# Optimization experiments

Hardware: AMD Instinct MI355X
Metric: run time of the kernel (lower is better)

Reference implementation:

```python
import jax, jax.numpy as jnp
import numpy as np

# Perfect-tree regularization of the recursive UpDownVec graph:
#   T tactics per internal node, S siblings per tactic, L levels, branching B = T*S.
T, S, L = 2, 4, 7
B = T * S
DIM = 128
EPS = 1.0  # epsilon in AggChildrenVec
SIZES = [B ** l for l in range(L)]          # nodes per level: 1, 8, ..., 262144
OFFS = np.concatenate([[0], np.cumsum(SIZES)])
N_TOTAL = int(OFFS[-1])                      # 299593


def setup_inputs() -> dict:
    key = jax.random.key(0)
    ks = jax.random.split(key, 12)
    sc = 1.0 / np.sqrt(DIM)
    return {
        "initial_vecs": jax.random.normal(ks[0], (N_TOTAL, DIM), jnp.float32),
        "Ws": jax.random.normal(ks[1], (DIM, DIM), jnp.float32) * sc,
        "bs": jax.random.normal(ks[2], (DIM,), jnp.float32) * sc,
        "Wc": jax.random.normal(ks[3], (DIM, DIM), jnp.float32) * sc,
        "bc": jax.random.normal(ks[4], (DIM,), jnp.float32) * sc,
        "Wx": jax.random.normal(ks[5], (DIM, DIM), jnp.float32) * sc,
        "bx": jax.random.normal(ks[6], (DIM,), jnp.float32) * sc,
        "Wf": jax.random.normal(ks[7], (DIM, 2 * DIM), jnp.float32) * sc,
        "bf": jax.random.normal(ks[8], (DIM,), jnp.float32) * sc,
        "Wh": jax.random.normal(ks[9], (1, DIM), jnp.float32) * sc,
        "bh": jax.random.normal(ks[10], (1,), jnp.float32) * sc,
    }


def reference(initial_vecs, Ws, bs, Wc, bc, Wx, bx, Wf, bf, Wh, bh):
    dim = initial_vecs.shape[-1]
    init = [initial_vecs[OFFS[l]:OFFS[l + 1]] for l in range(L)]  # static slices

    # ---- up_step (bottom-up): leaves -> root ----
    agg = [None] * L
    agg[L - 1] = init[L - 1]                                    # leaves: agg = initial
    for l in range(L - 2, -1, -1):
        ch = agg[l + 1].reshape(SIZES[l], T, S, dim)            # children agg vecs
        # AggSiblingsVec: mean over siblings of relu(linear)
        sib_h = jax.nn.relu(jnp.einsum('ntsd,ed->ntse', ch, Ws) + bs)
        sib_agg = sib_h.mean(axis=2)                            # [n, T, dim]
        # AggChildrenVec: node + eps * mean over tactics of relu(linear)
        ch_h = jax.nn.relu(jnp.einsum('ntd,ed->nte', sib_agg, Wc) + bc)
        agg[l] = init[l] + EPS * ch_h.mean(axis=1)

    # ---- down_step (top-down): root -> leaves ----
    ctx = [None] * L
    ctx[0] = jnp.ones((1, dim), initial_vecs.dtype)             # root context = ones
    for l in range(L - 1):
        # AggContextVec over cat([parent_ctx, other_siblings_agg]); mean is
        # order-invariant so set-based sibling gathering is reproduced exactly.
        h = jax.nn.relu(agg[l + 1] @ Wx.T + bx).reshape(SIZES[l], T, S, dim)
        sum_h = h.sum(axis=2)                                   # [n, T, dim]
        ctx_h = jax.nn.relu(ctx[l] @ Wx.T + bx)                 # [n, dim]
        child_ctx = (ctx_h[:, None, None, :] + sum_h[:, :, None, :] - h) / S
        ctx[l + 1] = child_ctx.reshape(SIZES[l + 1], dim)

    # ---- final_agg for every node ----
    ctx_all = jnp.concatenate(ctx, axis=0)                      # [N, dim]
    agg_all = jnp.concatenate(agg, axis=0)                      # [N, dim]
    x = jnp.concatenate([ctx_all, agg_all], axis=1)             # [N, 2*dim]
    x = jax.nn.relu(x @ Wf.T + bf)
    return x @ Wh.T + bh                                        # [N, 1]
```

## Files before the change

### kernel.cpp

```cpp
#include <hip/hip_runtime.h>
#include <stdint.h>

#define DIM 128

static constexpr long long NTOT = 299593LL;

using bf16x8 = __attribute__((ext_vector_type(8))) __bf16;
using f32x4  = __attribute__((ext_vector_type(4))) float;

__device__ __forceinline__ float relu(float x){ return x > 0.f ? x : 0.f; }
__device__ __forceinline__ __bf16 tobf(float x){ return (__bf16)x; }

__device__ __forceinline__ void mfma_acc(f32x4& acc, bf16x8 a, bf16x8 b){
    acc = __builtin_amdgcn_mfma_f32_16x16x32_bf16(a, b, acc, 0, 0, 0);
}

__device__ __forceinline__ int swz(int row, int col){
    return row*128 + (col ^ ((row & 7) << 3));
}

__global__ __launch_bounds__(256) void prep_kernel(
    const float* __restrict__ Ws, const float* __restrict__ Wc,
    const float* __restrict__ Wx, const float* __restrict__ Wf,
    __bf16* __restrict__ wfm, __bf16* __restrict__ ctx)
{
    int idx = blockIdx.x*256 + threadIdx.x;
    if (idx < 81920){
        int sel = idx >> 14;
        int d   = idx & 16383;
        int j = d & 7, ln = (d >> 3) & 63, f = d >> 9;
        int r = (f >> 2)*16 + (ln & 15);
        int c = (f & 3)*32 + (ln >> 4)*8 + j;
        float v;
        if      (sel == 0) v = Ws[r*128 + c];
        else if (sel == 1) v = Wc[r*128 + c];
        else if (sel == 2) v = Wx[r*128 + c];
        else if (sel == 3) v = Wf[r*256 + c];
        else               v = Wf[r*256 + 128 + c];
        wfm[idx] = tobf(v);
    } else if (idx < 82048){
        ctx[idx - 81920] = tobf(1.0f);
    }
}


__device__ __forceinline__ void up_level_task(
    const __bf16* __restrict__ lds_w,
    __bf16* __restrict__ sib,
    const float* __restrict__ init,
    const float* __restrict__ bsr, const float* __restrict__ bcr,
    __bf16* __restrict__ agg,
    long long task, long long cb, long long pb, long long n_par,
    int lane, int quad, int l15)
{
    const long long n_child = n_par*8;
    const long long c0 = task*64;
    bf16x8 af[4][4];
    #pragma unroll
    for (int tt = 0; tt < 4; ++tt){
        long long r = c0 + tt*16 + l15;
        if (r >= n_child) r = n_child - 1;
        const __bf16* p = agg + (cb + r)*DIM + quad*8;
        #pragma unroll
        for (int ks = 0; ks < 4; ++ks)
            af[tt][ks] = *(const bf16x8*)(p + ks*32);
    }
    #pragma unroll
    for (int h = 0; h < 2; ++h){
        f32x4 acc[2][8];
        #pragma unroll
        for (int u = 0; u < 2; ++u)
            #pragma unroll
            for (int i = 0; i < 8; ++i) acc[u][i] = f32x4{0.f,0.f,0.f,0.f};
        #pragma unroll
        for (int ks = 0; ks < 4; ++ks){
            #pragma unroll
            for (int nt = 0; nt < 8; ++nt){
                bf16x8 b = *(const bf16x8*)&lds_w[((nt*4+ks)<<9) + lane*8];
                mfma_acc(acc[0][nt], af[2*h+0][ks], b);
                mfma_acc(acc[1][nt], af[2*h+1][ks], b);
            }
        }
        #pragma unroll
        for (int u = 0; u < 2; ++u){
            const int row = (2*h+u)*4 + quad;
            #pragma unroll
            for (int nt = 0; nt < 8; ++nt){
                float b = bsr[nt];
                float s = relu(acc[u][nt][0]+b) + relu(acc[u][nt][1]+b)
                        + relu(acc[u][nt][2]+b) + relu(acc[u][nt][3]+b);
                sib[swz(row, nt*16 + l15)] = tobf(s*0.25f);
            }
        }
    }
    bf16x8 a2[4];
    #pragma unroll
    for (int ks = 0; ks < 4; ++ks)
        a2[ks] = *(const bf16x8*)&sib[swz(l15, ks*32 + quad*8)];
    f32x4 ac2[8];
    #pragma unroll
    for (int i = 0; i < 8; ++i) ac2[i] = f32x4{0.f,0.f,0.f,0.f};
    #pragma unroll
    for (int ks = 0; ks < 4; ++ks){
        #pragma unroll
        for (int nt = 0; nt < 8; ++nt){
            bf16x8 b = *(const bf16x8*)&lds_w[16384 + ((nt*4+ks)<<9) + lane*8];
            mfma_acc(ac2[nt], a2[ks], b);
        }
    }
    const long long p0l = task*8 + quad*2, p1l = p0l + 1;
    #pragma unroll
    for (int nt = 0; nt < 8; ++nt){
        int col = nt*16 + l15;
        float b = bcr[nt];
        float r0_ = relu(ac2[nt][0]+b), r1_ = relu(ac2[nt][1]+b);
        float r2_ = relu(ac2[nt][2]+b), r3_ = relu(ac2[nt][3]+b);
        if (p0l < n_par){
            long long gr = pb + p0l;
            agg[gr*DIM + col] = tobf(init[gr*DIM + col] + 0.5f*(r0_+r1_));
        }
        if (p1l < n_par){
            long long gr = pb + p1l;
            agg[gr*DIM + col] = tobf(init[gr*DIM + col] + 0.5f*(r2_+r3_));
        }
    }
}

__device__ __forceinline__ void down_level_task(
    const __bf16* __restrict__ lds_w,
    __bf16* __restrict__ ch,
    const float* __restrict__ bxr,
    const __bf16* __restrict__ agg, __bf16* __restrict__ ctx,
    long long task, long long pb, long long cb, long long n_par,
    int lane, int quad, int l15)
{
    const long long n_child = n_par*8;
    {
        long long p = task*16 + l15;
        if (p >= n_par) p = n_par - 1;
        bf16x8 ap[4];
        #pragma unroll
        for (int ks = 0; ks < 4; ++ks)
            ap[ks] = *(const bf16x8*)(ctx + (pb + p)*DIM + ks*32 + quad*8);
        f32x4 acp[8];
        #pragma unroll
        for (int i = 0; i < 8; ++i) acp[i] = f32x4{0.f,0.f,0.f,0.f};
        #pragma unroll
        for (int ks = 0; ks < 4; ++ks){
            #pragma unroll
            for (int nt = 0; nt < 8; ++nt){
                bf16x8 b = *(const bf16x8*)&lds_w[((nt*4+ks)<<9) + lane*8];
                mfma_acc(acp[nt], ap[ks], b);
            }
        }
        #pragma unroll
        for (int nt = 0; nt < 8; ++nt){
            float b = bxr[nt];
            #pragma unroll
            for (int rg = 0; rg < 4; ++rg)
                ch[swz(quad*4 + rg, nt*16 + l15)] = tobf(relu(acp[nt][rg] + b));
        }
    }
    #pragma unroll 1
    for (int ct = 0; ct < 8; ++ct){
        const long long ch0 = task*128 + ct*16;
        if (ch0 >= n_child) break;
        bf16x8 a[4];
        {
            long long r = ch0 + l15;
            if (r >= n_child) r = n_child - 1;
            const __bf16* p = agg + (cb + r)*DIM + quad*8;
            #pragma unroll
            for (int ks = 0; ks < 4; ++ks)
                a[ks] = *(const bf16x8*)(p + ks*32);
        }
        f32x4 acc[8];
        #pragma unroll
        for (int i = 0; i < 8; ++i) acc[i] = f32x4{0.f,0.f,0.f,0.f};
        #pragma unroll
        for (int ks = 0; ks < 4; ++ks){
            #pragma unroll
            for (int nt = 0; nt < 8; ++nt){
                bf16x8 b = *(const bf16x8*)&lds_w[((nt*4+ks)<<9) + lane*8];
                mfma_acc(acc[nt], a[ks], b);
            }
        }
        const long long rb = ch0 + quad*4;
        const int p_loc = ct*2 + (quad >> 1);
        #pragma unroll
        for (int nt = 0; nt < 8; ++nt){
            int col = nt*16 + l15;
            float b = bxr[nt];
            float h0 = relu(acc[nt][0]+b), h1 = relu(acc[nt][1]+b);
            float h2 = relu(acc[nt][2]+b), h3 = relu(acc[nt][3]+b);
            float s = h0 + h1 + h2 + h3;
            float chv = (float)ch[swz(p_loc, col)];
            if (rb   < n_child) ctx[(cb + rb  )*DIM + col] = tobf((chv + s - h0)*0.25f);
            if (rb+1 < n_child) ctx[(cb + rb+1)*DIM + col] = tobf((chv + s - h1)*0.25f);
            if (rb+2 < n_child) ctx[(cb + rb+2)*DIM + col] = tobf((chv + s - h2)*0.25f);
            if (rb+3 < n_child) ctx[(cb + rb+3)*DIM + col] = tobf((chv + s - h3)*0.25f);
        }
    }
}

__global__ __launch_bounds__(256, 2) void upleaf_kernel(
    const __bf16* __restrict__ wfm,
    const float* __restrict__ init,
    const float* __restrict__ bs, const float* __restrict__ bc,
    __bf16* __restrict__ agg)
{
    __shared__ __attribute__((aligned(16))) __bf16 lds_w[32768];
    __shared__ __attribute__((aligned(16))) __bf16 lds_sib[4*2048];
    {
        const int t = threadIdx.x;
        #pragma unroll
        for (int i = 0; i < 16; ++i){
            int c = i*256 + t;
            *((uint4*)lds_w + c) = *((const uint4*)wfm + c);
        }
    }
    __syncthreads();

    const int t = threadIdx.x, w = t>>6, lane = t&63, quad = lane>>4, l15 = lane&15;
    const int sboff = w*2048;

    float bsr[8], bcr[8];
    #pragma unroll
    for (int nt = 0; nt < 8; ++nt){ bsr[nt] = bs[nt*16 + l15]; bcr[nt] = bc[nt*16 + l15]; }

    const long long gw = blockIdx.x*4 + w;
    const long long r0 = gw*64;
    const long long cb = 37449LL;
    const long long pb = 4681LL + gw*8;

    const long long pr0 = pb + quad*2, pr1 = pr0 + 1;
    float pinit0[8], pinit1[8];
    #pragma unroll
    for (int nt = 0; nt < 8; ++nt){
        pinit0[nt] = init[pr0*DIM + nt*16 + l15];
        pinit1[nt] = init[pr1*DIM + nt*16 + l15];
    }

    bf16x8 af[4][4];
    #pragma unroll
    for (int tt = 0; tt < 4; ++tt){
        const long long base = (cb + r0 + tt*16 + l15)*DIM + quad*8;
        const float* p = init + base;
        #pragma unroll
        for (int ks = 0; ks < 4; ++ks){
            float4 v0 = *(const float4*)(p + ks*32);
            float4 v1 = *(const float4*)(p + ks*32 + 4);
            bf16x8 a;
            a[0]=tobf(v0.x); a[1]=tobf(v0.y); a[2]=tobf(v0.z); a[3]=tobf(v0.w);
            a[4]=tobf(v1.x); a[5]=tobf(v1.y); a[6]=tobf(v1.z); a[7]=tobf(v1.w);
            af[tt][ks] = a;
            *(uint4*)(agg + base + ks*32) = *(uint4*)&a;
        }
    }

    #pragma unroll
    for (int h = 0; h < 2; ++h){
        f32x4 acc[2][8];
        #pragma unroll
        for (int u = 0; u < 2; ++u)
            #pragma unroll
            for (int i = 0; i < 8; ++i) acc[u][i] = f32x4{0.f,0.f,0.f,0.f};
        #pragma unroll
        for (int ks = 0; ks < 4; ++ks){
            #pragma unroll
            for (int nt = 0; nt < 8; ++nt){
                bf16x8 b = *(const bf16x8*)&lds_w[((nt*4+ks)<<9) + lane*8];
                mfma_acc(acc[0][nt], af[2*h+0][ks], b);
                mfma_acc(acc[1][nt], af[2*h+1][ks], b);
            }
        }
        #pragma unroll
        for (int u = 0; u < 2; ++u){
            const int row = (2*h+u)*4 + quad;
            #pragma unroll
            for (int nt = 0; nt < 8; ++nt){
                float b = bsr[nt];
                float s = relu(acc[u][nt][0]+b) + relu(acc[u][nt][1]+b)
                        + relu(acc[u][nt][2]+b) + relu(acc[u][nt][3]+b);
                lds_sib[sboff + swz(row, nt*16 + l15)] = tobf(s*0.25f);
            }
        }
    }

    bf16x8 a2[4];
    #pragma unroll
    for (int ks = 0; ks < 4; ++ks)
        a2[ks] = *(const bf16x8*)&lds_sib[sboff + swz(l15, ks*32 + quad*8)];
    f32x4 ac2[8];
    #pragma unroll
    for (int i = 0; i < 8; ++i) ac2[i] = f32x4{0.f,0.f,0.f,0.f};
    #pragma unroll
    for (int ks = 0; ks < 4; ++ks){
        #pragma unroll
        for (int nt = 0; nt < 8; ++nt){
            bf16x8 b = *(const bf16x8*)&lds_w[16384 + ((nt*4+ks)<<9) + lane*8];
            mfma_acc(ac2[nt], a2[ks], b);
        }
    }
    #pragma unroll
    for (int nt = 0; nt < 8; ++nt){
        int col = nt*16 + l15;
        float b = bcr[nt];
        float r0_ = relu(ac2[nt][0]+b), r1_ = relu(ac2[nt][1]+b);
        float r2_ = relu(ac2[nt][2]+b), r3_ = relu(ac2[nt][3]+b);
        agg[pr0*DIM + col] = tobf(pinit0[nt] + 0.5f*(r0_+r1_));
        agg[pr1*DIM + col] = tobf(pinit1[nt] + 0.5f*(r2_+r3_));
    }
}

__global__ __launch_bounds__(256, 2) void up_mid_kernel(
    const __bf16* __restrict__ wfm, const float* __restrict__ init,
    const float* __restrict__ bs, const float* __restrict__ bc,
    __bf16* __restrict__ agg,
    long long cb, long long pb, long long n_par)
{
    __shared__ __attribute__((aligned(16))) __bf16 lds_w[32768];
    __shared__ __attribute__((aligned(16))) __bf16 lds_sib[4*2048];
    {
        const int t = threadIdx.x;
        #pragma unroll
        for (int i = 0; i < 16; ++i)
            ((uint4*)lds_w)[i*256 + t] = ((const uint4*)wfm)[i*256 + t];
    }
    __syncthreads();
    const int t = threadIdx.x, w = t>>6, lane = t&63, quad = lane>>4, l15 = lane&15;
    float bsr[8], bcr[8];
    #pragma unroll
    for (int nt = 0; nt < 8; ++nt){ bsr[nt] = bs[nt*16 + l15]; bcr[nt] = bc[nt*16 + l15]; }
    const long long task = (long long)blockIdx.x*4 + w;
    if (task*8 < n_par)
        up_level_task(lds_w, lds_sib + w*2048, init, bsr, bcr, agg,
                      task, cb, pb, n_par, lane, quad, l15);
}

__global__ __launch_bounds__(512, 2) void up_tail_kernel(
    const __bf16* __restrict__ wfm, const float* __restrict__ init,
    const float* __restrict__ bs, const float* __restrict__ bc,
    __bf16* __restrict__ agg)
{
    __shared__ __attribute__((aligned(16))) __bf16 lds_w[32768];
    __shared__ __attribute__((aligned(16))) __bf16 lds_sib[8*2048];
    {
        const int t = threadIdx.x;
        #pragma unroll
        for (int i = 0; i < 8; ++i)
            ((uint4*)lds_w)[i*512 + t] = ((const uint4*)wfm)[i*512 + t];
    }
    __syncthreads();
    const int t = threadIdx.x, w = t>>6, lane = t&63, quad = lane>>4, l15 = lane&15;
    float bsr[8], bcr[8];
    #pragma unroll
    for (int nt = 0; nt < 8; ++nt){ bsr[nt] = bs[nt*16 + l15]; bcr[nt] = bc[nt*16 + l15]; }
    __bf16* sib = lds_sib + w*2048;
    if (w < 8) up_level_task(lds_w, sib, init, bsr, bcr, agg, w, 73, 9, 64, lane, quad, l15);
    __syncthreads();
    if (w == 0) up_level_task(lds_w, sib, init, bsr, bcr, agg, 0, 9, 1, 8, lane, quad, l15);
    __syncthreads();
    if (w == 0) up_level_task(lds_w, sib, init, bsr, bcr, agg, 0, 1, 0, 1, lane, quad, l15);
}

__global__ __launch_bounds__(512, 2) void down_tail_kernel(
    const __bf16* __restrict__ wfm,
    const float* __restrict__ bx,
    const __bf16* __restrict__ agg, __bf16* __restrict__ ctx)
{
    __shared__ __attribute__((aligned(16))) __bf16 lds_w[16384];
    __shared__ __attribute__((aligned(16))) __bf16 lds_ch[8*2048];
    {
        const int t = threadIdx.x;
        #pragma unroll
        for (int i = 0; i < 4; ++i)
            ((uint4*)lds_w)[i*512 + t] = ((const uint4*)wfm)[i*512 + t];
    }
    __syncthreads();
    const int t = threadIdx.x, w = t>>6, lane = t&63, quad = lane>>4, l15 = lane&15;
    float bxr[8];
    #pragma unroll
    for (int nt = 0; nt < 8; ++nt) bxr[nt] = bx[nt*16 + l15];
    __bf16* ch = lds_ch + w*2048;
    if (w == 0) down_level_task(lds_w, ch, bxr, agg, ctx, 0, 0, 1, 1, lane, quad, l15);
    __syncthreads();
    if (w == 0) down_level_task(lds_w, ch, bxr, agg, ctx, 0, 1, 9, 8, lane, quad, l15);
    __syncthreads();
    if (w < 4) down_level_task(lds_w, ch, bxr, agg, ctx, w, 9, 73, 64, lane, quad, l15);
}

__global__ __launch_bounds__(256, 2) void down_mid_kernel(
    const __bf16* __restrict__ wfm,
    const float* __restrict__ bx,
    const __bf16* __restrict__ agg, __bf16* __restrict__ ctx,
    long long pb, long long cb, long long n_par)
{
    __shared__ __attribute__((aligned(16))) __bf16 lds_w[16384];
    __shared__ __attribute__((aligned(16))) __bf16 lds_ch[4*2048];
    {
        const int t = threadIdx.x;
        #pragma unroll
        for (int i = 0; i < 8; ++i)
            ((uint4*)lds_w)[i*256 + t] = ((const uint4*)wfm)[i*256 + t];
    }
    __syncthreads();
    const int t = threadIdx.x, w = t>>6, lane = t&63, quad = lane>>4, l15 = lane&15;
    float bxr[8];
    #pragma unroll
    for (int nt = 0; nt < 8; ++nt) bxr[nt] = bx[nt*16 + l15];
    const long long task = (long long)blockIdx.x*4 + w;
    if (task*16 < n_par)
        down_level_task(lds_w, lds_ch + w*2048, bxr, agg, ctx,
                        task, pb, cb, n_par, lane, quad, l15);
}

__global__ __launch_bounds__(512, 2) void downfinal_kernel(
    const __bf16* __restrict__ wx,
    const __bf16* __restrict__ wf,
    const float* __restrict__ bx, const float* __restrict__ bf_,
    const float* __restrict__ Wh, const float* __restrict__ bh,
    const __bf16* __restrict__ agg, const __bf16* __restrict__ ctx,
    float* __restrict__ out)
{
    __shared__ __attribute__((aligned(16))) __bf16 lds_wx[16384];
    __shared__ __attribute__((aligned(16))) __bf16 lds_wf[32768];
    __shared__ __attribute__((aligned(16))) __bf16 lds_st[8*2048];
    {
        const int t = threadIdx.x;
        #pragma unroll
        for (int i = 0; i < 4; ++i)
            ((uint4*)lds_wx)[i*512+t] = ((const uint4*)wx)[i*512+t];
        #pragma unroll
        for (int i = 0; i < 8; ++i)
            ((uint4*)lds_wf)[i*512+t] = ((const uint4*)wf)[i*512+t];
    }
    __syncthreads();

    const int t = threadIdx.x, w = t>>6, lane = t&63, quad = lane>>4, l15 = lane&15;
    const int stoff = w*2048;
    const long long task = (long long)blockIdx.x*8 + w;
    const long long cb = 37449LL;
    const long long pg = 4681LL + task*16;

    float bxr[8], bfr[8], whr[8];
    #pragma unroll
    for (int nt = 0; nt < 8; ++nt){
        bxr[nt] = bx[nt*16 + l15];
        bfr[nt] = bf_[nt*16 + l15];
        whr[nt] = Wh[nt*16 + l15];
    }
    const float bb = bh[0];

    float chv[8][4];
    {
        bf16x8 ap[4];
        #pragma unroll
        for (int ks = 0; ks < 4; ++ks)
            ap[ks] = *(const bf16x8*)(ctx + (pg + l15)*DIM + ks*32 + quad*8);
        f32x4 acp[8];
        #pragma unroll
        for (int i = 0; i < 8; ++i) acp[i] = f32x4{0.f,0.f,0.f,0.f};
        #pragma unroll
        for (int ks = 0; ks < 4; ++ks){
            #pragma unroll
            for (int nt = 0; nt < 8; ++nt){
                bf16x8 b = *(const bf16x8*)&lds_wx[((nt*4+ks)<<9) + lane*8];
                mfma_acc(acp[nt], ap[ks], b);
            }
        }
        #pragma unroll
        for (int nt = 0; nt < 8; ++nt){
            #pragma unroll
            for (int rg = 0; rg < 4; ++rg)
                chv[nt][rg] = relu(acp[nt][rg] + bxr[nt]);
        }
    }

#define DF_TILE(CT, P, AF)                                                      \
    {                                                                           \
        f32x4 acch[8];                                                          \
        _Pragma("unroll") for (int i = 0; i < 8; ++i) acch[i] = f32x4{0.f,0.f,0.f,0.f}; \
        _Pragma("unroll") for (int ks = 0; ks < 4; ++ks){                       \
            _Pragma("unroll") for (int nt = 0; nt < 8; ++nt){                   \
                bf16x8 b = *(const bf16x8*)&lds_wx[((nt*4+ks)<<9) + lane*8];    \
                mfma_acc(acch[nt], AF[ks], b);                                  \
            }                                                                   \
        }                                                                       \
        const int srcl = ((CT)>>1)*16 + l15;                                    \
        _Pragma("unroll") for (int nt = 0; nt < 8; ++nt){                       \
            float vA = __shfl(chv[nt][2*(P)],   srcl);                          \
            float vB = __shfl(chv[nt][2*(P)+1], srcl);                          \
            float ch = (quad >= 2) ? vB : vA;                                   \
            float b = bxr[nt];                                                  \
            float h0 = relu(acch[nt][0]+b), h1 = relu(acch[nt][1]+b);           \
            float h2 = relu(acch[nt][2]+b), h3 = relu(acch[nt][3]+b);           \
            float s = h0+h1+h2+h3;                                              \
            int col = nt*16 + l15;                                              \
            lds_st[stoff + swz(quad*4+0, col)] = tobf((ch+s-h0)*0.25f);         \
            lds_st[stoff + swz(quad*4+1, col)] = tobf((ch+s-h1)*0.25f);         \
            lds_st[stoff + swz(quad*4+2, col)] = tobf((ch+s-h2)*0.25f);         \
            lds_st[stoff + swz(quad*4+3, col)] = tobf((ch+s-h3)*0.25f);         \
        }                                                                       \
        bf16x8 cf[4];                                                           \
        _Pragma("unroll") for (int ks = 0; ks < 4; ++ks)                        \
            cf[ks] = *(const bf16x8*)&lds_st[stoff + swz(l15, ks*32 + quad*8)]; \
        f32x4 accf[8];                                                          \
        _Pragma("unroll") for (int i = 0; i < 8; ++i) accf[i] = f32x4{0.f,0.f,0.f,0.f}; \
        _Pragma("unroll") for (int ks = 0; ks < 4; ++ks){                       \
            _Pragma("unroll") for (int nt = 0; nt < 8; ++nt){                   \
                bf16x8 b0 = *(const bf16x8*)&lds_wf[((nt*4+ks)<<9) + lane*8];           \
                bf16x8 b1 = *(const bf16x8*)&lds_wf[16384 + ((nt*4+ks)<<9) + lane*8];   \
                mfma_acc(accf[nt], cf[ks], b0);                                 \
                mfma_acc(accf[nt], AF[ks], b1);                                 \
            }                                                                   \
        }                                                                       \
        float p0=0.f,p1=0.f,p2=0.f,p3=0.f;                                      \
        _Pragma("unroll") for (int nt = 0; nt < 8; ++nt){                       \
            float b = bfr[nt], wh = whr[nt];                                    \
            p0 += relu(accf[nt][0]+b)*wh; p1 += relu(accf[nt][1]+b)*wh;         \
            p2 += relu(accf[nt][2]+b)*wh; p3 += relu(accf[nt][3]+b)*wh;         \
        }                                                                       \
        _Pragma("unroll") for (int m = 1; m < 16; m <<= 1){                     \
            p0 += __shfl_xor(p0, m); p1 += __shfl_xor(p1, m);                   \
            p2 += __shfl_xor(p2, m); p3 += __shfl_xor(p3, m);                   \
        }                                                                       \
        if (l15 == 0){                                                          \
            long long r = cb + task*128 + (long long)(CT)*16 + quad*4;          \
            out[r] = p0 + bb; out[r+1] = p1 + bb;                               \
            out[r+2] = p2 + bb; out[r+3] = p3 + bb;                             \
        }                                                                       \
    }

    auto LOADA = [&](bf16x8* d, int ct){
        const __bf16* p = agg + (cb + task*128 + ct*16 + l15)*DIM + quad*8;
        #pragma unroll
        for (int ks = 0; ks < 4; ++ks) d[ks] = *(const bf16x8*)(p + ks*32);
    };

    bf16x8 aA[4], aB[4];
    LOADA(aA, 0);
    #pragma unroll 1
    for (int cp = 0; cp < 4; ++cp){
        const int ct0 = cp*2, ct1 = ct0 + 1;
        LOADA(aB, ct1);
        DF_TILE(ct0, 0, aA);
        if (cp < 3) LOADA(aA, ct0 + 2);
        DF_TILE(ct1, 1, aB);
    }
#undef DF_TILE
}

__global__ __launch_bounds__(512, 2) void final_nl_kernel(
    const __bf16* __restrict__ wfm,
    const __bf16* __restrict__ ctx, const __bf16* __restrict__ agg,
    const float* __restrict__ bf_,
    const float* __restrict__ Wh, const float* __restrict__ bh,
    float* __restrict__ out, long long nrows)
{
    __shared__ __attribute__((aligned(16))) __bf16 lds_w[32768];
    {
        const int t = threadIdx.x;
        #pragma unroll
        for (int i = 0; i < 8; ++i){
            int c = i*512 + t;
            *((uint4*)lds_w + c) = *((const uint4*)wfm + c);
        }
    }
    __syncthreads();
    const int t = threadIdx.x, w = t>>6, lane = t&63, quad = lane>>4, l15 = lane&15;
    float bfr[8], whr[8];
    #pragma unroll
    for (int nt = 0; nt < 8; ++nt){
        bfr[nt] = bf_[nt*16 + l15];
        whr[nt] = Wh[nt*16 + l15];
    }
    const float bb = bh[0];
    const long long stride = (long long)gridDim.x*8;
    #pragma unroll 1
    for (long long tile = blockIdx.x*8 + w; ; tile += stride){
        const long long r0 = tile*32;
        if (r0 >= nrows) break;
        f32x4 acc[2][8];
        #pragma unroll
        for (int tt = 0; tt < 2; ++tt)
            #pragma unroll
            for (int i = 0; i < 8; ++i) acc[tt][i] = f32x4{0.f,0.f,0.f,0.f};
        #pragma unroll
        for (int half = 0; half < 2; ++half){
            const __bf16* src = half ? agg : ctx;
            bf16x8 a[2][4];
            #pragma unroll
            for (int tt = 0; tt < 2; ++tt){
                long long r = r0 + tt*16 + l15;
                if (r >= nrows) r = nrows - 1;
                #pragma unroll
                for (int ks = 0; ks < 4; ++ks)
                    a[tt][ks] = *(const bf16x8*)(src + r*DIM + ks*32 + quad*8);
            }
            #pragma unroll
            for (int ks = 0; ks < 4; ++ks){
                #pragma unroll
                for (int nt = 0; nt < 8; ++nt){
                    bf16x8 b = *(const bf16x8*)&lds_w[half*16384 + ((nt*4+ks)<<9) + lane*8];
                    mfma_acc(acc[0][nt], a[0][ks], b);
                    mfma_acc(acc[1][nt], a[1][ks], b);
                }
            }
        }
        #pragma unroll
        for (int tt = 0; tt < 2; ++tt){
            float p0 = 0.f, p1 = 0.f, p2 = 0.f, p3 = 0.f;
            #pragma unroll
            for (int nt = 0; nt < 8; ++nt){
                float b = bfr[nt], wh = whr[nt];
                p0 += relu(acc[tt][nt][0]+b)*wh;
                p1 += relu(acc[tt][nt][1]+b)*wh;
                p2 += relu(acc[tt][nt][2]+b)*wh;
                p3 += relu(acc[tt][nt][3]+b)*wh;
            }
            #pragma unroll
            for (int m = 1; m < 16; m <<= 1){
                p0 += __shfl_xor(p0, m);
                p1 += __shfl_xor(p1, m);
                p2 += __shfl_xor(p2, m);
                p3 += __shfl_xor(p3, m);
            }
            if (l15 == 0){
                long long r = r0 + tt*16 + quad*4;
                if (r   < nrows) out[r  ] = p0 + bb;
                if (r+1 < nrows) out[r+1] = p1 + bb;
                if (r+2 < nrows) out[r+2] = p2 + bb;
                if (r+3 < nrows) out[r+3] = p3 + bb;
            }
        }
    }
}

extern "C" void kernel_launch(void* const* d_in, const int* in_sizes, int n_in,
                              void* d_out, int out_size, void* d_ws, size_t ws_size,
                              hipStream_t stream)
{
    const float* init = (const float*)d_in[0];
    const float* Ws  = (const float*)d_in[1];
    const float* bs  = (const float*)d_in[2];
    const float* Wc  = (const float*)d_in[3];
    const float* bc  = (const float*)d_in[4];
    const float* Wx  = (const float*)d_in[5];
    const float* bx  = (const float*)d_in[6];
    const float* Wf  = (const float*)d_in[7];
    const float* bff = (const float*)d_in[8];
    const float* Wh  = (const float*)d_in[9];
    const float* bh  = (const float*)d_in[10];
    float* out = (float*)d_out;

    __bf16* agg = (__bf16*)d_ws;
    __bf16* ctx = agg + NTOT*DIM;
    __bf16* wfm = ctx + NTOT*DIM;

    prep_kernel<<<dim3(321), dim3(256), 0, stream>>>(Ws, Wc, Wx, Wf, wfm, ctx);

    upleaf_kernel<<<dim3(1024), dim3(256), 0, stream>>>(wfm, init, bs, bc, agg);
    up_mid_kernel<<<dim3(128), dim3(256), 0, stream>>>(wfm, init, bs, bc, agg,
                                                       4681LL, 585LL, 4096LL);
    up_mid_kernel<<<dim3(16), dim3(256), 0, stream>>>(wfm, init, bs, bc, agg,
                                                      585LL, 73LL, 512LL);
    up_tail_kernel<<<dim3(1), dim3(512), 0, stream>>>(wfm, init, bs, bc, agg);

    down_tail_kernel<<<dim3(1), dim3(512), 0, stream>>>(wfm + 32768, bx, agg, ctx);
    down_mid_kernel<<<dim3(8), dim3(256), 0, stream>>>(wfm + 32768, bx, agg, ctx,
                                                       73LL, 585LL, 512LL);
    down_mid_kernel<<<dim3(64), dim3(256), 0, stream>>>(wfm + 32768, bx, agg, ctx,
                                                        585LL, 4681LL, 4096LL);
    downfinal_kernel<<<dim3(256), dim3(512), 0, stream>>>(
        wfm + 32768, wfm + 49152, bx, bff, Wh, bh, agg, ctx, out);
    final_nl_kernel<<<dim3(147), dim3(512), 0, stream>>>(
        wfm + 49152, ctx, agg, bff, Wh, bh, out, 37449LL);
}
```

Before: 426.1 us.

## Halve leaf-kernel LDS weight buffer for higher occupancy; deepen prefetch in leaf down kernel

The leaf up kernel now keeps only one 128x128 weight matrix in LDS at a time. It loads Ws first and reloads Wc after the sibling stage, with extra barriers, and raises launch bounds to 3 blocks per CU. The intent is to cut LDS use so more blocks stay resident and hide global latency. The leaf down/final kernel now issues the parent ctx load and four agg tile loads up front and fully unrolls the 8 tiles with a 4-deep prefetch, replacing the 2-deep loop. This adds register pressure, which could spill or offset the occupancy gain.

```diff
diff --git a/kernel.cpp b/kernel.cpp
--- a/kernel.cpp
+++ b/kernel.cpp
@@ -203,25 +203,22 @@
     }
 }
 
-__global__ __launch_bounds__(256, 2) void upleaf_kernel(
+__global__ __launch_bounds__(256, 3) void upleaf_kernel(
     const __bf16* __restrict__ wfm,
     const float* __restrict__ init,
     const float* __restrict__ bs, const float* __restrict__ bc,
     __bf16* __restrict__ agg)
 {
-    __shared__ __attribute__((aligned(16))) __bf16 lds_w[32768];
+    __shared__ __attribute__((aligned(16))) __bf16 lds_w[16384];
     __shared__ __attribute__((aligned(16))) __bf16 lds_sib[4*2048];
-    {
-        const int t = threadIdx.x;
-        #pragma unroll
-        for (int i = 0; i < 16; ++i){
-            int c = i*256 + t;
-            *((uint4*)lds_w + c) = *((const uint4*)wfm + c);
-        }
-    }
-    __syncthreads();
-
-    const int t = threadIdx.x, w = t>>6, lane = t&63, quad = lane>>4, l15 = lane&15;
+    const int t = threadIdx.x;
+    {
+        #pragma unroll
+        for (int i = 0; i < 8; ++i)
+            ((uint4*)lds_w)[i*256 + t] = ((const uint4*)wfm)[i*256 + t];
+    }
+
+    const int w = t>>6, lane = t&63, quad = lane>>4, l15 = lane&15;
     const int sboff = w*2048;
 
     float bsr[8], bcr[8];
@@ -240,6 +237,7 @@
         pinit0[nt] = init[pr0*DIM + nt*16 + l15];
         pinit1[nt] = init[pr1*DIM + nt*16 + l15];
     }
+    __syncthreads();
 
     bf16x8 af[4][4];
     #pragma unroll
@@ -286,6 +284,13 @@
             }
         }
     }
+    __syncthreads();
+    {
+        #pragma unroll
+        for (int i = 0; i < 8; ++i)
+            ((uint4*)lds_w)[i*256 + t] = ((const uint4*)(wfm + 16384))[i*256 + t];
+    }
+    __syncthreads();
 
     bf16x8 a2[4];
     #pragma unroll
@@ -298,7 +303,7 @@
     for (int ks = 0; ks < 4; ++ks){
         #pragma unroll
         for (int nt = 0; nt < 8; ++nt){
-            bf16x8 b = *(const bf16x8*)&lds_w[16384 + ((nt*4+ks)<<9) + lane*8];
+            bf16x8 b = *(const bf16x8*)&lds_w[((nt*4+ks)<<9) + lane*8];
             mfma_acc(ac2[nt], a2[ks], b);
         }
     }
@@ -452,12 +457,21 @@
     }
     const float bb = bh[0];
 
+    auto LOADA = [&](bf16x8* d, int ct){
+        const __bf16* p = agg + (cb + task*128 + ct*16 + l15)*DIM + quad*8;
+        #pragma unroll
+        for (int ks = 0; ks < 4; ++ks) d[ks] = *(const bf16x8*)(p + ks*32);
+    };
+
+    bf16x8 ap[4];
+    #pragma unroll
+    for (int ks = 0; ks < 4; ++ks)
+        ap[ks] = *(const bf16x8*)(ctx + (pg + l15)*DIM + ks*32 + quad*8);
+    bf16x8 a0[4], a1[4], a2t[4], a3[4];
+    LOADA(a0, 0); LOADA(a1, 1); LOADA(a2t, 2); LOADA(a3, 3);
+
     float chv[8][4];
     {
-        bf16x8 ap[4];
-        #pragma unroll
-        for (int ks = 0; ks < 4; ++ks)
-            ap[ks] = *(const bf16x8*)(ctx + (pg + l15)*DIM + ks*32 + quad*8);
         f32x4 acp[8];
         #pragma unroll
         for (int i = 0; i < 8; ++i) acp[i] = f32x4{0.f,0.f,0.f,0.f};
@@ -532,22 +546,14 @@
         }                                                                       \
     }
 
-    auto LOADA = [&](bf16x8* d, int ct){
-        const __bf16* p = agg + (cb + task*128 + ct*16 + l15)*DIM + quad*8;
-        #pragma unroll
-        for (int ks = 0; ks < 4; ++ks) d[ks] = *(const bf16x8*)(p + ks*32);
-    };
-
-    bf16x8 aA[4], aB[4];
-    LOADA(aA, 0);
-    #pragma unroll 1
-    for (int cp = 0; cp < 4; ++cp){
-        const int ct0 = cp*2, ct1 = ct0 + 1;
-        LOADA(aB, ct1);
-        DF_TILE(ct0, 0, aA);
-        if (cp < 3) LOADA(aA, ct0 + 2);
-        DF_TILE(ct1, 1, aB);
-    }
+    DF_TILE(0, 0, a0);  LOADA(a0, 4);
+    DF_TILE(1, 1, a1);  LOADA(a1, 5);
+    DF_TILE(2, 0, a2t); LOADA(a2t, 6);
+    DF_TILE(3, 1, a3);  LOADA(a3, 7);
+    DF_TILE(4, 0, a0);
+    DF_TILE(5, 1, a1);
+    DF_TILE(6, 0, a2t);
+    DF_TILE(7, 1, a3);
 #undef DF_TILE
 }
 
```

Measured after the change: 452.8 us. +6.3%, slower.

## Fuse small up/down tree levels into cooperative kernels and drop leaf agg writes

Applied to the files above, without the earlier changes.

Replaces the three up-pass launches for levels 4..0 and the three down-pass launches for levels 0..4 with one cooperative kernel each, using grid-wide syncs between levels instead of separate kernel launches. It also stops writing bf16 leaf agg values to global memory. The final leaf kernel instead reads and converts the fp32 initial vectors directly. This cuts launch overhead and about 67MB of bf16 writes, but adds grid.sync cost and roughly twice the leaf read traffic in downfinal.

```diff
diff --git a/kernel.cpp b/kernel.cpp
--- a/kernel.cpp
+++ b/kernel.cpp
@@ -1,5 +1,8 @@
 #include <hip/hip_runtime.h>
+#include <hip/hip_cooperative_groups.h>
 #include <stdint.h>
+
+namespace cg = cooperative_groups;
 
 #define DIM 128
 
@@ -254,7 +257,6 @@
             a[0]=tobf(v0.x); a[1]=tobf(v0.y); a[2]=tobf(v0.z); a[3]=tobf(v0.w);
             a[4]=tobf(v1.x); a[5]=tobf(v1.y); a[6]=tobf(v1.z); a[7]=tobf(v1.w);
             af[tt][ks] = a;
-            *(uint4*)(agg + base + ks*32) = *(uint4*)&a;
         }
     }
 
@@ -313,12 +315,13 @@
     }
 }
 
-__global__ __launch_bounds__(256, 2) void up_mid_kernel(
-    const __bf16* __restrict__ wfm, const float* __restrict__ init,
+__global__ __launch_bounds__(256, 2) void up_small_kernel(
+    const __bf16* __restrict__ wfm,
+    const float* __restrict__ init,
     const float* __restrict__ bs, const float* __restrict__ bc,
-    __bf16* __restrict__ agg,
-    long long cb, long long pb, long long n_par)
-{
+    __bf16* __restrict__ agg)
+{
+    cg::grid_group grid = cg::this_grid();
     __shared__ __attribute__((aligned(16))) __bf16 lds_w[32768];
     __shared__ __attribute__((aligned(16))) __bf16 lds_sib[4*2048];
     {
@@ -328,74 +331,34 @@
             ((uint4*)lds_w)[i*256 + t] = ((const uint4*)wfm)[i*256 + t];
     }
     __syncthreads();
+
     const int t = threadIdx.x, w = t>>6, lane = t&63, quad = lane>>4, l15 = lane&15;
+    const int nblk = gridDim.x;
+    const long long gw = (long long)w*nblk + blockIdx.x;
+
     float bsr[8], bcr[8];
     #pragma unroll
     for (int nt = 0; nt < 8; ++nt){ bsr[nt] = bs[nt*16 + l15]; bcr[nt] = bc[nt*16 + l15]; }
-    const long long task = (long long)blockIdx.x*4 + w;
-    if (task*8 < n_par)
-        up_level_task(lds_w, lds_sib + w*2048, init, bsr, bcr, agg,
-                      task, cb, pb, n_par, lane, quad, l15);
-}
-
-__global__ __launch_bounds__(512, 2) void up_tail_kernel(
-    const __bf16* __restrict__ wfm, const float* __restrict__ init,
-    const float* __restrict__ bs, const float* __restrict__ bc,
-    __bf16* __restrict__ agg)
-{
-    __shared__ __attribute__((aligned(16))) __bf16 lds_w[32768];
-    __shared__ __attribute__((aligned(16))) __bf16 lds_sib[8*2048];
-    {
-        const int t = threadIdx.x;
-        #pragma unroll
-        for (int i = 0; i < 8; ++i)
-            ((uint4*)lds_w)[i*512 + t] = ((const uint4*)wfm)[i*512 + t];
-    }
-    __syncthreads();
-    const int t = threadIdx.x, w = t>>6, lane = t&63, quad = lane>>4, l15 = lane&15;
-    float bsr[8], bcr[8];
-    #pragma unroll
-    for (int nt = 0; nt < 8; ++nt){ bsr[nt] = bs[nt*16 + l15]; bcr[nt] = bc[nt*16 + l15]; }
-    __bf16* sib = lds_sib + w*2048;
-    if (w < 8) up_level_task(lds_w, sib, init, bsr, bcr, agg, w, 73, 9, 64, lane, quad, l15);
-    __syncthreads();
-    if (w == 0) up_level_task(lds_w, sib, init, bsr, bcr, agg, 0, 9, 1, 8, lane, quad, l15);
-    __syncthreads();
-    if (w == 0) up_level_task(lds_w, sib, init, bsr, bcr, agg, 0, 1, 0, 1, lane, quad, l15);
-}
-
-__global__ __launch_bounds__(512, 2) void down_tail_kernel(
+
+    #pragma unroll 1
+    for (int l = 4; l >= 0; --l){
+        const long long n_par = 1LL << (3*l);
+        const long long cb = ((1LL << (3*(l+1))) - 1)/7;
+        const long long pb = ((1LL << (3*l)) - 1)/7;
+        const long long ntask = (n_par + 7) >> 3;
+        if (gw < ntask)
+            up_level_task(lds_w, lds_sib + w*2048, init, bsr, bcr, agg,
+                          gw, cb, pb, n_par, lane, quad, l15);
+        if (l > 0) grid.sync();
+    }
+}
+
+__global__ __launch_bounds__(256, 2) void down_small_kernel(
     const __bf16* __restrict__ wfm,
     const float* __restrict__ bx,
     const __bf16* __restrict__ agg, __bf16* __restrict__ ctx)
 {
-    __shared__ __attribute__((aligned(16))) __bf16 lds_w[16384];
-    __shared__ __attribute__((aligned(16))) __bf16 lds_ch[8*2048];
-    {
-        const int t = threadIdx.x;
-        #pragma unroll
-        for (int i = 0; i < 4; ++i)
-            ((uint4*)lds_w)[i*512 + t] = ((const uint4*)wfm)[i*512 + t];
-    }
-    __syncthreads();
-    const int t = threadIdx.x, w = t>>6, lane = t&63, quad = lane>>4, l15 = lane&15;
-    float bxr[8];
-    #pragma unroll
-    for (int nt = 0; nt < 8; ++nt) bxr[nt] = bx[nt*16 + l15];
-    __bf16* ch = lds_ch + w*2048;
-    if (w == 0) down_level_task(lds_w, ch, bxr, agg, ctx, 0, 0, 1, 1, lane, quad, l15);
-    __syncthreads();
-    if (w == 0) down_level_task(lds_w, ch, bxr, agg, ctx, 0, 1, 9, 8, lane, quad, l15);
-    __syncthreads();
-    if (w < 4) down_level_task(lds_w, ch, bxr, agg, ctx, w, 9, 73, 64, lane, quad, l15);
-}
-
-__global__ __launch_bounds__(256, 2) void down_mid_kernel(
-    const __bf16* __restrict__ wfm,
-    const float* __restrict__ bx,
-    const __bf16* __restrict__ agg, __bf16* __restrict__ ctx,
-    long long pb, long long cb, long long n_par)
-{
+    cg::grid_group grid = cg::this_grid();
     __shared__ __attribute__((aligned(16))) __bf16 lds_w[16384];
     __shared__ __attribute__((aligned(16))) __bf16 lds_ch[4*2048];
     {
@@ -405,14 +368,26 @@
             ((uint4*)lds_w)[i*256 + t] = ((const uint4*)wfm)[i*256 + t];
     }
     __syncthreads();
+
     const int t = threadIdx.x, w = t>>6, lane = t&63, quad = lane>>4, l15 = lane&15;
+    const int nblk = gridDim.x;
+    const long long gw = (long long)w*nblk + blockIdx.x;
+
     float bxr[8];
     #pragma unroll
     for (int nt = 0; nt < 8; ++nt) bxr[nt] = bx[nt*16 + l15];
-    const long long task = (long long)blockIdx.x*4 + w;
-    if (task*16 < n_par)
-        down_level_task(lds_w, lds_ch + w*2048, bxr, agg, ctx,
-                        task, pb, cb, n_par, lane, quad, l15);
+
+    #pragma unroll 1
+    for (int l = 0; l < 5; ++l){
+        const long long n_par = 1LL << (3*l);
+        const long long pb = ((1LL << (3*l)) - 1)/7;
+        const long long cb = ((1LL << (3*(l+1))) - 1)/7;
+        const long long ntask = (n_par + 15) >> 4;
+        if (gw < ntask)
+            down_level_task(lds_w, lds_ch + w*2048, bxr, agg, ctx,
+                            gw, pb, cb, n_par, lane, quad, l15);
+        if (l < 4) grid.sync();
+    }
 }
 
 __global__ __launch_bounds__(512, 2) void downfinal_kernel(
@@ -420,7 +395,7 @@
     const __bf16* __restrict__ wf,
     const float* __restrict__ bx, const float* __restrict__ bf_,
     const float* __restrict__ Wh, const float* __restrict__ bh,
-    const __bf16* __restrict__ agg, const __bf16* __restrict__ ctx,
+    const float* __restrict__ init, const __bf16* __restrict__ ctx,
     float* __restrict__ out)
 {
     __shared__ __attribute__((aligned(16))) __bf16 lds_wx[16384];
@@ -533,9 +508,16 @@
     }
 
     auto LOADA = [&](bf16x8* d, int ct){
-        const __bf16* p = agg + (cb + task*128 + ct*16 + l15)*DIM + quad*8;
-        #pragma unroll
-        for (int ks = 0; ks < 4; ++ks) d[ks] = *(const bf16x8*)(p + ks*32);
+        const float* p = init + (cb + task*128 + ct*16 + l15)*DIM + quad*8;
+        #pragma unroll
+        for (int ks = 0; ks < 4; ++ks){
+            float4 v0 = *(const float4*)(p + ks*32);
+            float4 v1 = *(const float4*)(p + ks*32 + 4);
+            bf16x8 a;
+            a[0]=tobf(v0.x); a[1]=tobf(v0.y); a[2]=tobf(v0.z); a[3]=tobf(v0.w);
+            a[4]=tobf(v1.x); a[5]=tobf(v1.y); a[6]=tobf(v1.z); a[7]=tobf(v1.w);
+            d[ks] = a;
+        }
     };
 
     bf16x8 aA[4], aB[4];
@@ -657,23 +639,24 @@
     __bf16* agg = (__bf16*)d_ws;
     __bf16* ctx = agg + NTOT*DIM;
     __bf16* wfm = ctx + NTOT*DIM;
+    __bf16* wfm_dn = wfm + 32768;
+    __bf16* wfm_wf = wfm + 49152;
 
     prep_kernel<<<dim3(321), dim3(256), 0, stream>>>(Ws, Wc, Wx, Wf, wfm, ctx);
 
     upleaf_kernel<<<dim3(1024), dim3(256), 0, stream>>>(wfm, init, bs, bc, agg);
-    up_mid_kernel<<<dim3(128), dim3(256), 0, stream>>>(wfm, init, bs, bc, agg,
-                                                       4681LL, 585LL, 4096LL);
-    up_mid_kernel<<<dim3(16), dim3(256), 0, stream>>>(wfm, init, bs, bc, agg,
-                                                      585LL, 73LL, 512LL);
-    up_tail_kernel<<<dim3(1), dim3(512), 0, stream>>>(wfm, init, bs, bc, agg);
-
-    down_tail_kernel<<<dim3(1), dim3(512), 0, stream>>>(wfm + 32768, bx, agg, ctx);
-    down_mid_kernel<<<dim3(8), dim3(256), 0, stream>>>(wfm + 32768, bx, agg, ctx,
-                                                       73LL, 585LL, 512LL);
-    down_mid_kernel<<<dim3(64), dim3(256), 0, stream>>>(wfm + 32768, bx, agg, ctx,
-                                                        585LL, 4681LL, 4096LL);
+    {
+        void* args[] = {(void*)&wfm, (void*)&init, (void*)&bs, (void*)&bc, (void*)&agg};
+        hipLaunchCooperativeKernel((void*)up_small_kernel, dim3(256), dim3(256),
+                                   args, 0, stream);
+    }
+    {
+        void* args[] = {(void*)&wfm_dn, (void*)&bx, (void*)&agg, (void*)&ctx};
+        hipLaunchCooperativeKernel((void*)down_small_kernel, dim3(256), dim3(256),
+                                   args, 0, stream);
+    }
     downfinal_kernel<<<dim3(256), dim3(512), 0, stream>>>(
-        wfm + 32768, wfm + 49152, bx, bff, Wh, bh, agg, ctx, out);
+        wfm_dn, wfm_wf, bx, bff, Wh, bh, init, ctx, out);
     final_nl_kernel<<<dim3(147), dim3(512), 0, stream>>>(
-        wfm + 49152, ctx, agg, bff, Wh, bh, out, 37449LL);
-}
+        wfm_wf, ctx, agg, bff, Wh, bh, out, 37449LL);
+}
```

New measurement: 665.2 us. +56.1%, slower.
